# Performance work log

Measured on AMD Instinct MI355X. Metric: run time of the kernel, lower is better.

## Reference

```python
import jax, jax.numpy as jnp
import numpy as np
import math

B, T, C = 4, 2048, 1024
H = 16
D = C // H

def setup_inputs() -> dict:
    key = jax.random.key(0)
    k1, k2, k3 = jax.random.split(key, 3)
    x = jax.random.normal(k1, (B, T, C), dtype=jnp.float32)
    w_attn = jax.random.normal(k2, (3 * C, C), dtype=jnp.float32) * (1.0 / math.sqrt(C))
    b_attn = jnp.zeros((3 * C,), dtype=jnp.float32)
    w_proj = jax.random.normal(k3, (C, C), dtype=jnp.float32) * (1.0 / math.sqrt(C))
    b_proj = jnp.zeros((C,), dtype=jnp.float32)
    return {"x": x, "w_attn": w_attn, "b_attn": b_attn, "w_proj": w_proj, "b_proj": b_proj}

def reference(x, w_attn, b_attn, w_proj, b_proj):
    Bq, Tq, Cq = x.shape
    qkv = x @ w_attn.T + b_attn                      # [B,T,3C]
    q, k, v = jnp.split(qkv, 3, axis=-1)
    q = q.reshape(Bq, Tq, H, D).transpose(0, 2, 1, 3)  # [B,H,T,D]
    k = k.reshape(Bq, Tq, H, D).transpose(0, 2, 1, 3)
    v = v.reshape(Bq, Tq, H, D).transpose(0, 2, 1, 3)
    att = jnp.einsum('bhqd,bhkd->bhqk', q, k) * (1.0 / math.sqrt(D))
    causal = jnp.tril(jnp.ones((Tq, Tq), dtype=bool))
    att = jnp.where(causal[None, None], att, -jnp.inf)
    att = jax.nn.softmax(att, axis=-1)
    y = jnp.einsum('bhqk,bhkd->bhqd', att, v)          # [B,H,T,D]
    y = y.transpose(0, 2, 1, 3).reshape(Bq, Tq, Cq)
    return y @ w_proj.T + b_proj
```

## Files before the change

### kernel.cpp

```cpp
#include <hip/hip_runtime.h>
#include <hip/hip_bf16.h>


typedef __hip_bfloat16 bf16;
typedef __attribute__((ext_vector_type(8))) short bf16x8;
typedef __attribute__((ext_vector_type(4))) float f32x4;
typedef __attribute__((ext_vector_type(16))) float f32x16;

#define MFMA16(a, b, c) __builtin_amdgcn_mfma_f32_16x16x32_bf16(a, b, c, 0, 0, 0)
#define MFMA32(a, b, c) __builtin_amdgcn_mfma_f32_32x32x16_bf16(a, b, c, 0, 0, 0)
#define GLOAD_LDS(g, l) __builtin_amdgcn_global_load_lds( \
    (const __attribute__((address_space(1))) void*)(g),    \
    (__attribute__((address_space(3))) void*)(l), 16, 0, 0)

constexpr int Bn = 4, Tn = 2048, Cn = 1024, Hn = 16, Dn = 64;
constexpr size_t HT_ELEMS = (size_t)64 * Tn * Dn;
constexpr float QSCALE = 0.18033688011112042f;

__device__ __forceinline__ short f2bf(float f) {
    unsigned u = __float_as_uint(f);
    return (short)((u + 0x7FFF + ((u >> 16) & 1)) >> 16);
}
__device__ __forceinline__ bf16 bfbits(short s) { bf16 b; __builtin_memcpy(&b, &s, 2); return b; }

__device__ __forceinline__ unsigned cvtpk_bf16(float lo, float hi) {
    unsigned r;
    asm("v_cvt_pk_bf16_f32 %0, %1, %2" : "=v"(r) : "v"(lo), "v"(hi));
    return r;
}
__device__ __forceinline__ void permswap(unsigned& a, unsigned& b) {
#if __has_builtin(__builtin_amdgcn_permlane32_swap)
    auto r = __builtin_amdgcn_permlane32_swap(a, b, false, false);
    a = (unsigned)r[0]; b = (unsigned)r[1];
#else
    asm("v_permlane32_swap_b32 %0, %1" : "+v"(a), "+v"(b));
#endif
}
__device__ __forceinline__ bf16x8 pack4(unsigned w0, unsigned w1, unsigned w2, unsigned w3) {
    union { unsigned u[4]; bf16x8 v; } t;
    t.u[0] = w0; t.u[1] = w1; t.u[2] = w2; t.u[3] = w3;
    return t.v;
}

__global__ __launch_bounds__(256) void cast3_kernel(
    const float* __restrict__ x, const float* __restrict__ wa,
    const float* __restrict__ wp, bf16* __restrict__ out)
{
    size_t i = (size_t)blockIdx.x * 256 + threadIdx.x;
    const float* src; size_t off;
    if (i < 1048576)      { src = x;  off = i; }
    else if (i < 1441792) { src = wa; off = i - 1048576; }
    else                  { src = wp; off = i - 1441792; }
    const float4* p = (const float4*)(src + off * 8);
    float4 a = p[0], b = p[1];
    bf16x8 r;
    r[0] = f2bf(a.x); r[1] = f2bf(a.y); r[2] = f2bf(a.z); r[3] = f2bf(a.w);
    r[4] = f2bf(b.x); r[5] = f2bf(b.y); r[6] = f2bf(b.z); r[7] = f2bf(b.w);
    *(bf16x8*)(out + i * 8) = r;
}

__global__ __launch_bounds__(256) void qkv_gemm128(
    const bf16* __restrict__ Am, const bf16* __restrict__ Wm,
    const float* __restrict__ bias,
    bf16* __restrict__ qo, bf16* __restrict__ ko, bf16* __restrict__ vo)
{
    constexpr int K = 1024;
    __shared__ bf16 As[4096], Bs[4096];
    const int tid = threadIdx.x;
    const int lane = tid & 63, w = tid >> 6;
    const int row = lane & 15, quad = lane >> 4;
    const int tn = blockIdx.x % 24, tm = blockIdx.x / 24;
    const int m0 = tm * 128, n0 = tn * 128;

    const int srow = tid >> 2, skch = tid & 3;
    const bf16* ag0 = Am + (size_t)(m0 + srow) * K + skch * 8;
    const bf16* ag1 = ag0 + (size_t)64 * K;
    const bf16* wg0 = Wm + (size_t)(n0 + srow) * K + skch * 8;
    const bf16* wg1 = wg0 + (size_t)64 * K;
    bf16* asl0 = As + tid * 8;  bf16* asl1 = As + 2048 + tid * 8;
    bf16* bsl0 = Bs + tid * 8;  bf16* bsl1 = Bs + 2048 + tid * 8;

    f32x4 acc[4][4];
    #pragma unroll
    for (int i = 0; i < 4; i++)
        #pragma unroll
        for (int j = 0; j < 4; j++) acc[i][j] = {0, 0, 0, 0};

    const int r0 = (w >> 1) * 64, c0 = (w & 1) * 64;

    for (int k0 = 0; k0 < K; k0 += 32) {
        __syncthreads();
        GLOAD_LDS(ag0 + k0, asl0);
        GLOAD_LDS(ag1 + k0, asl1);
        GLOAD_LDS(wg0 + k0, bsl0);
        GLOAD_LDS(wg1 + k0, bsl1);
        __syncthreads();
        bf16x8 af[4], bfv[4];
        #pragma unroll
        for (int it = 0; it < 4; it++)
            af[it] = *(const bf16x8*)(As + (r0 + it * 16 + row) * 32 + quad * 8);
        #pragma unroll
        for (int jt = 0; jt < 4; jt++)
            bfv[jt] = *(const bf16x8*)(Bs + (c0 + jt * 16 + row) * 32 + quad * 8);
        #pragma unroll
        for (int it = 0; it < 4; it++)
            #pragma unroll
            for (int jt = 0; jt < 4; jt++)
                acc[it][jt] = MFMA16(af[it], bfv[jt], acc[it][jt]);
    }

    #pragma unroll
    for (int it = 0; it < 4; it++)
    #pragma unroll
    for (int jt = 0; jt < 4; jt++)
    #pragma unroll
    for (int r = 0; r < 4; r++) {
        int m = m0 + r0 + it * 16 + quad * 4 + r;
        int n = n0 + c0 + jt * 16 + row;
        float val = acc[it][jt][r] + bias[n];
        int which = n >> 10, cc = n & 1023;
        if (which == 0) val *= QSCALE;
        bf16 bv = bfbits(f2bf(val));
        int h = cc >> 6, d = cc & 63;
        int b = m >> 11, t = m & 2047;
        int bh = b * Hn + h;
        if (which == 0)      qo[((size_t)bh * Tn + t) * Dn + d] = bv;
        else if (which == 1) ko[((size_t)bh * Tn + t) * Dn + d] = bv;
        else                 vo[((size_t)bh * 64 + (t >> 5)) * 2048 + (size_t)d * 32 + (t & 31)] = bv;
    }
}

__global__ __launch_bounds__(256, 4) void attn_kernel(
    const bf16* __restrict__ qbp, const bf16* __restrict__ kbp,
    const bf16* __restrict__ vtb, bf16* __restrict__ ob,
    unsigned* __restrict__ counters)
{
    __shared__ __align__(128) bf16 SB[4][2048];
    __shared__ float lbufw[4][32];
    __shared__ unsigned item_s;
    const int tid  = threadIdx.x;
    const int lane = tid & 63;
    const int w    = tid >> 6;
    const int l31  = lane & 31, hl = lane >> 5;
    const int qid  = blockIdx.x & 7;
    unsigned* ctr  = counters + qid * 32;

    const int stage_off = w * 1024 + (lane >> 3) * 128
                        + (((lane & 7) ^ ((lane >> 3) & 7)) << 4);
    const int kxor = (l31 & 7) << 4;
    const int sxor = ((l31 >> 1) & 7) << 4;

    for (;;) {
        if (tid == 0) item_s = atomicAdd(ctr, 1u);
        __syncthreads();
        const unsigned item = item_s;
        if (item >= 128u) break;
        const int qb8  = 15 - (int)(item >> 3);
        const int bh   = qid * 8 + (int)(item & 7);
        const int jmax = qb8 * 4 + 3;
        const int qtw  = qb8 * 4 + w;
        const int q0w  = qtw * 32;

        const bf16* Q  = qbp + (size_t)bh * Tn * Dn;
        const char* Kh = (const char*)(kbp + (size_t)bh * Tn * Dn);
        const char* Vh = (const char*)vtb + (size_t)bh * 262144;

        bf16x8 bQ[4];
        {
            const bf16* qp = Q + (size_t)(q0w + l31) * Dn + hl * 8;
            #pragma unroll
            for (int kf = 0; kf < 4; kf++) bQ[kf] = *(const bf16x8*)(qp + kf * 16);
        }

        f32x16 o2[2];
        o2[0] = {0,0,0,0,0,0,0,0,0,0,0,0,0,0,0,0};
        o2[1] = {0,0,0,0,0,0,0,0,0,0,0,0,0,0,0,0};
        float lsum = 0.f;

        GLOAD_LDS(Kh + stage_off, (char*)SB[0] + w * 1024);
        GLOAD_LDS(Vh + stage_off, (char*)SB[2] + w * 1024);
        __syncthreads();

        for (int j = 0; j <= jmax; j++) {
            const int cur = j & 1;
            if (j < jmax) {
                const int nb = cur ^ 1;
                GLOAD_LDS(Kh + (size_t)(j + 1) * 4096 + stage_off, (char*)SB[nb] + w * 1024);
                GLOAD_LDS(Vh + (size_t)(j + 1) * 4096 + stage_off, (char*)SB[2 + nb] + w * 1024);
            }
            if (j <= qtw) {
                const char* KB = (const char*)SB[cur];
                const char* VB = (const char*)SB[2 + cur];
                bf16x8 aK[4];
                #pragma unroll
                for (int kf = 0; kf < 4; kf++)
                    aK[kf] = *(const bf16x8*)(KB + l31 * 128 + ((((kf * 2 + hl)) << 4) ^ kxor));

                f32x16 s = {0,0,0,0,0,0,0,0,0,0,0,0,0,0,0,0};
                __builtin_amdgcn_s_setprio(1);
                s = MFMA32(aK[0], bQ[0], s);
                s = MFMA32(aK[1], bQ[1], s);
                s = MFMA32(aK[2], bQ[2], s);
                s = MFMA32(aK[3], bQ[3], s);
                __builtin_amdgcn_s_setprio(0);

                bf16x8 vf[4];
                #pragma unroll
                for (int i2 = 0; i2 < 4; i2++) {
                    const int vh = i2 >> 1, kc = i2 & 1;
                    const int stripe = vh * 16 + (l31 >> 1);
                    vf[i2] = *(const bf16x8*)(VB + stripe * 128
                              + ((((l31 & 1) * 4 + kc * 2 + hl) << 4) ^ sxor));
                }

                float p[16];
                if (j == qtw) {
                    #pragma unroll
                    for (int r = 0; r < 16; r++) {
                        const int krow = (r & 3) + 8 * (r >> 2) + 4 * hl;
                        float e = exp2f(s[r]);
                        p[r] = (krow > l31) ? 0.f : e;
                    }
                } else {
                    #pragma unroll
                    for (int r = 0; r < 16; r++) p[r] = exp2f(s[r]);
                }
                lsum += (((p[0]+p[1]) + (p[2]+p[3])) + ((p[4]+p[5]) + (p[6]+p[7])))
                      + (((p[8]+p[9]) + (p[10]+p[11])) + ((p[12]+p[13]) + (p[14]+p[15])));

                unsigned a0 = cvtpk_bf16(p[0],  p[1]),  b0 = cvtpk_bf16(p[4],  p[5]);
                unsigned a1 = cvtpk_bf16(p[2],  p[3]),  b1 = cvtpk_bf16(p[6],  p[7]);
                unsigned a2 = cvtpk_bf16(p[8],  p[9]),  b2 = cvtpk_bf16(p[12], p[13]);
                unsigned a3 = cvtpk_bf16(p[10], p[11]), b3 = cvtpk_bf16(p[14], p[15]);
                permswap(a0, b0);
                permswap(a1, b1);
                permswap(a2, b2);
                permswap(a3, b3);
                const bf16x8 P0 = pack4(a0, a1, b0, b1);
                const bf16x8 P1 = pack4(a2, a3, b2, b3);

                __builtin_amdgcn_s_setprio(1);
                o2[0] = MFMA32(P0, vf[0], o2[0]);
                o2[0] = MFMA32(P1, vf[1], o2[0]);
                o2[1] = MFMA32(P0, vf[2], o2[1]);
                o2[1] = MFMA32(P1, vf[3], o2[1]);
                __builtin_amdgcn_s_setprio(0);
            }
            __syncthreads();
        }

        unsigned lsu = __float_as_uint(lsum), lsv = lsu;
        permswap(lsu, lsv);
        const float ltot = __uint_as_float(lsu) + __uint_as_float(lsv);
        if (hl == 0) lbufw[w][l31] = 1.0f / ltot;
        asm volatile("s_waitcnt lgkmcnt(0)" ::: "memory");

        char* obl = (char*)SB[w];
        #pragma unroll
        for (int r = 0; r < 16; r++) {
            const int q  = (r & 3) + 8 * (r >> 2) + 4 * hl;
            const float rl = lbufw[w][q];
            const int qx = (q & 7) << 4;
            *(short*)(obl + q * 128 + ((2 * l31) ^ qx))      = f2bf(o2[0][r] * rl);
            *(short*)(obl + q * 128 + ((64 + 2 * l31) ^ qx)) = f2bf(o2[1][r] * rl);
        }
        asm volatile("s_waitcnt lgkmcnt(0)" ::: "memory");

        {
            const int q = lane >> 1, half = lane & 1;
            const int qx = (q & 7) << 4;
            const int b = bh >> 4, h = bh & 15;
            bf16* gdst = ob + ((size_t)(b * Tn + (q0w + q))) * Cn + h * Dn + half * 32;
            #pragma unroll
            for (int c = 0; c < 4; c++) {
                bf16x8 rv = *(const bf16x8*)(obl + q * 128 + (((half * 64) + c * 16) ^ qx));
                *(bf16x8*)(gdst + c * 8) = rv;
            }
        }
        __syncthreads();
    }
}

__global__ __launch_bounds__(256) void proj_gemm128(
    const bf16* __restrict__ Am, const bf16* __restrict__ Wm,
    const float* __restrict__ bias, float* __restrict__ out)
{
    constexpr int K = 1024;
    __shared__ bf16 As[4096], Bs[4096];
    const int tid = threadIdx.x;
    const int lane = tid & 63, w = tid >> 6;
    const int row = lane & 15, quad = lane >> 4;
    const int tn = blockIdx.x % 8, tm = blockIdx.x / 8;
    const int m0 = tm * 128, n0 = tn * 128;

    const int srow = tid >> 2, skch = tid & 3;
    const bf16* ag0 = Am + (size_t)(m0 + srow) * K + skch * 8;
    const bf16* ag1 = ag0 + (size_t)64 * K;
    const bf16* wg0 = Wm + (size_t)(n0 + srow) * K + skch * 8;
    const bf16* wg1 = wg0 + (size_t)64 * K;
    bf16* asl0 = As + tid * 8;  bf16* asl1 = As + 2048 + tid * 8;
    bf16* bsl0 = Bs + tid * 8;  bf16* bsl1 = Bs + 2048 + tid * 8;

    f32x4 acc[4][4];
    #pragma unroll
    for (int i = 0; i < 4; i++)
        #pragma unroll
        for (int j = 0; j < 4; j++) acc[i][j] = {0, 0, 0, 0};

    const int r0 = (w >> 1) * 64, c0 = (w & 1) * 64;

    for (int k0 = 0; k0 < K; k0 += 32) {
        __syncthreads();
        GLOAD_LDS(ag0 + k0, asl0);
        GLOAD_LDS(ag1 + k0, asl1);
        GLOAD_LDS(wg0 + k0, bsl0);
        GLOAD_LDS(wg1 + k0, bsl1);
        __syncthreads();
        bf16x8 af[4], bfv[4];
        #pragma unroll
        for (int it = 0; it < 4; it++)
            af[it] = *(const bf16x8*)(As + (r0 + it * 16 + row) * 32 + quad * 8);
        #pragma unroll
        for (int jt = 0; jt < 4; jt++)
            bfv[jt] = *(const bf16x8*)(Bs + (c0 + jt * 16 + row) * 32 + quad * 8);
        #pragma unroll
        for (int it = 0; it < 4; it++)
            #pragma unroll
            for (int jt = 0; jt < 4; jt++)
                acc[it][jt] = MFMA16(af[it], bfv[jt], acc[it][jt]);
    }

    #pragma unroll
    for (int it = 0; it < 4; it++)
    #pragma unroll
    for (int jt = 0; jt < 4; jt++)
    #pragma unroll
    for (int r = 0; r < 4; r++) {
        int m = m0 + r0 + it * 16 + quad * 4 + r;
        int n = n0 + c0 + jt * 16 + row;
        out[(size_t)m * 1024 + n] = acc[it][jt][r] + bias[n];
    }
}

extern "C" void kernel_launch(void* const* d_in, const int* in_sizes, int n_in,
                              void* d_out, int out_size, void* d_ws, size_t ws_size,
                              hipStream_t stream) {
    const float* x      = (const float*)d_in[0];
    const float* w_attn = (const float*)d_in[1];
    const float* b_attn = (const float*)d_in[2];
    const float* w_proj = (const float*)d_in[3];
    const float* b_proj = (const float*)d_in[4];
    float* out = (float*)d_out;

    unsigned* counters = (unsigned*)d_ws;
    bf16* ws  = (bf16*)((char*)d_ws + 1024);
    bf16* xb  = ws;
    bf16* wab = xb  + (size_t)8192 * 1024;
    bf16* wpb = wab + (size_t)3072 * 1024;
    bf16* q   = wpb + (size_t)1024 * 1024;
    bf16* k   = q  + HT_ELEMS;
    bf16* vt  = k  + HT_ELEMS;
    bf16* o   = vt + HT_ELEMS;

    hipMemsetAsync(counters, 0, 1024, stream);

    cast3_kernel<<<6144, 256, 0, stream>>>(x, w_attn, w_proj, xb);

    qkv_gemm128 <<<64 * 24, 256, 0, stream>>>(xb, wab, b_attn, q, k, vt);
    attn_kernel <<<1024, 256, 0, stream>>>(q, k, vt, o, counters);
    proj_gemm128<<<64 * 8, 256, 0, stream>>>(o, wpb, b_proj, out);
}
```

Before: 304.7 us.

## Double-buffer LDS tiles and swizzle block order in QKV and projection GEMMs

Both GEMM kernels now keep two LDS buffers, prefetching the next K-slice with global_load_lds while MFMAs consume the current one. This cuts the k-loop from two barriers to one and is meant to overlap memory latency with compute. Block indices are also remapped with an XCD-style swizzle (bid&7 groups) to improve L2 locality across the MI355X chiplets. LDS use doubles, which may lower occupancy, and the async-load completion ordering relies on the single barrier at the end of each iteration.

```diff
diff --git a/kernel.cpp b/kernel.cpp
--- a/kernel.cpp
+++ b/kernel.cpp
@@ -65,11 +65,13 @@
     bf16* __restrict__ qo, bf16* __restrict__ ko, bf16* __restrict__ vo)
 {
     constexpr int K = 1024;
-    __shared__ bf16 As[4096], Bs[4096];
+    __shared__ bf16 As[2][4096], Bs[2][4096];
     const int tid = threadIdx.x;
     const int lane = tid & 63, w = tid >> 6;
     const int row = lane & 15, quad = lane >> 4;
-    const int tn = blockIdx.x % 24, tm = blockIdx.x / 24;
+    const unsigned bid = blockIdx.x;
+    const unsigned swz = (bid & 7) * 192 + (bid >> 3);
+    const int tn = swz % 24, tm = swz / 24;
     const int m0 = tm * 128, n0 = tn * 128;
 
     const int srow = tid >> 2, skch = tid & 3;
@@ -77,8 +79,6 @@
     const bf16* ag1 = ag0 + (size_t)64 * K;
     const bf16* wg0 = Wm + (size_t)(n0 + srow) * K + skch * 8;
     const bf16* wg1 = wg0 + (size_t)64 * K;
-    bf16* asl0 = As + tid * 8;  bf16* asl1 = As + 2048 + tid * 8;
-    bf16* bsl0 = Bs + tid * 8;  bf16* bsl1 = Bs + 2048 + tid * 8;
 
     f32x4 acc[4][4];
     #pragma unroll
@@ -88,25 +88,37 @@
 
     const int r0 = (w >> 1) * 64, c0 = (w & 1) * 64;
 
+    GLOAD_LDS(ag0, As[0] + tid * 8);
+    GLOAD_LDS(ag1, As[0] + 2048 + tid * 8);
+    GLOAD_LDS(wg0, Bs[0] + tid * 8);
+    GLOAD_LDS(wg1, Bs[0] + 2048 + tid * 8);
+    __syncthreads();
+
+    int cur = 0;
     for (int k0 = 0; k0 < K; k0 += 32) {
-        __syncthreads();
-        GLOAD_LDS(ag0 + k0, asl0);
-        GLOAD_LDS(ag1 + k0, asl1);
-        GLOAD_LDS(wg0 + k0, bsl0);
-        GLOAD_LDS(wg1 + k0, bsl1);
-        __syncthreads();
+        const int nb = cur ^ 1;
+        if (k0 + 32 < K) {
+            GLOAD_LDS(ag0 + k0 + 32, As[nb] + tid * 8);
+            GLOAD_LDS(ag1 + k0 + 32, As[nb] + 2048 + tid * 8);
+            GLOAD_LDS(wg0 + k0 + 32, Bs[nb] + tid * 8);
+            GLOAD_LDS(wg1 + k0 + 32, Bs[nb] + 2048 + tid * 8);
+        }
+        const bf16* Ac = As[cur];
+        const bf16* Bc = Bs[cur];
         bf16x8 af[4], bfv[4];
         #pragma unroll
         for (int it = 0; it < 4; it++)
-            af[it] = *(const bf16x8*)(As + (r0 + it * 16 + row) * 32 + quad * 8);
+            af[it] = *(const bf16x8*)(Ac + (r0 + it * 16 + row) * 32 + quad * 8);
         #pragma unroll
         for (int jt = 0; jt < 4; jt++)
-            bfv[jt] = *(const bf16x8*)(Bs + (c0 + jt * 16 + row) * 32 + quad * 8);
+            bfv[jt] = *(const bf16x8*)(Bc + (c0 + jt * 16 + row) * 32 + quad * 8);
         #pragma unroll
         for (int it = 0; it < 4; it++)
             #pragma unroll
             for (int jt = 0; jt < 4; jt++)
                 acc[it][jt] = MFMA16(af[it], bfv[jt], acc[it][jt]);
+        __syncthreads();
+        cur = nb;
     }
 
     #pragma unroll
@@ -286,11 +298,13 @@
     const float* __restrict__ bias, float* __restrict__ out)
 {
     constexpr int K = 1024;
-    __shared__ bf16 As[4096], Bs[4096];
+    __shared__ bf16 As[2][4096], Bs[2][4096];
     const int tid = threadIdx.x;
     const int lane = tid & 63, w = tid >> 6;
     const int row = lane & 15, quad = lane >> 4;
-    const int tn = blockIdx.x % 8, tm = blockIdx.x / 8;
+    const unsigned bid = blockIdx.x;
+    const unsigned swz = (bid & 7) * 64 + (bid >> 3);
+    const int tn = swz % 8, tm = swz / 8;
     const int m0 = tm * 128, n0 = tn * 128;
 
     const int srow = tid >> 2, skch = tid & 3;
@@ -298,8 +312,6 @@
     const bf16* ag1 = ag0 + (size_t)64 * K;
     const bf16* wg0 = Wm + (size_t)(n0 + srow) * K + skch * 8;
     const bf16* wg1 = wg0 + (size_t)64 * K;
-    bf16* asl0 = As + tid * 8;  bf16* asl1 = As + 2048 + tid * 8;
-    bf16* bsl0 = Bs + tid * 8;  bf16* bsl1 = Bs + 2048 + tid * 8;
 
     f32x4 acc[4][4];
     #pragma unroll
@@ -309,25 +321,37 @@
 
     const int r0 = (w >> 1) * 64, c0 = (w & 1) * 64;
 
+    GLOAD_LDS(ag0, As[0] + tid * 8);
+    GLOAD_LDS(ag1, As[0] + 2048 + tid * 8);
+    GLOAD_LDS(wg0, Bs[0] + tid * 8);
+    GLOAD_LDS(wg1, Bs[0] + 2048 + tid * 8);
+    __syncthreads();
+
+    int cur = 0;
     for (int k0 = 0; k0 < K; k0 += 32) {
-        __syncthreads();
-        GLOAD_LDS(ag0 + k0, asl0);
-        GLOAD_LDS(ag1 + k0, asl1);
-        GLOAD_LDS(wg0 + k0, bsl0);
-        GLOAD_LDS(wg1 + k0, bsl1);
-        __syncthreads();
+        const int nb = cur ^ 1;
+        if (k0 + 32 < K) {
+            GLOAD_LDS(ag0 + k0 + 32, As[nb] + tid * 8);
+            GLOAD_LDS(ag1 + k0 + 32, As[nb] + 2048 + tid * 8);
+            GLOAD_LDS(wg0 + k0 + 32, Bs[nb] + tid * 8);
+            GLOAD_LDS(wg1 + k0 + 32, Bs[nb] + 2048 + tid * 8);
+        }
+        const bf16* Ac = As[cur];
+        const bf16* Bc = Bs[cur];
         bf16x8 af[4], bfv[4];
         #pragma unroll
         for (int it = 0; it < 4; it++)
-            af[it] = *(const bf16x8*)(As + (r0 + it * 16 + row) * 32 + quad * 8);
+            af[it] = *(const bf16x8*)(Ac + (r0 + it * 16 + row) * 32 + quad * 8);
         #pragma unroll
         for (int jt = 0; jt < 4; jt++)
-            bfv[jt] = *(const bf16x8*)(Bs + (c0 + jt * 16 + row) * 32 + quad * 8);
+            bfv[jt] = *(const bf16x8*)(Bc + (c0 + jt * 16 + row) * 32 + quad * 8);
         #pragma unroll
         for (int it = 0; it < 4; it++)
             #pragma unroll
             for (int jt = 0; jt < 4; jt++)
                 acc[it][jt] = MFMA16(af[it], bfv[jt], acc[it][jt]);
+        __syncthreads();
+        cur = nb;
     }
 
     #pragma unroll
```

After: 287.2 us. 5.7% less time.

## Replace atomic work queue with static paired causal tiles and XCD-aware block remap

Applied to the files above, without the earlier changes.

The attention kernel no longer takes work items from atomic counters. Each of 512 blocks now handles a fixed pair of query tiles (pair and 15-pair) for one head, which balances the causal workload statically and removes both the memset and the per-item atomics and syncs. Both GEMMs remap block indices so that blocks sharing the low 3 bits (likely the same XCD under round-robin dispatch) work on contiguous tiles, aiming for better L2 reuse. The static schedule gives up the dynamic load balancing the queue provided, and the new attention grid of 512 blocks may leave compute units underused if occupancy is limited.

```diff
diff --git a/kernel.cpp b/kernel.cpp
--- a/kernel.cpp
+++ b/kernel.cpp
@@ -69,7 +69,10 @@
     const int tid = threadIdx.x;
     const int lane = tid & 63, w = tid >> 6;
     const int row = lane & 15, quad = lane >> 4;
-    const int tn = blockIdx.x % 24, tm = blockIdx.x / 24;
+    const unsigned bid = blockIdx.x;
+    const int x8 = bid & 7, l = bid >> 3;
+    const int tm = (x8 >> 1) * 16 + l / 12;
+    const int tn = (x8 & 1) * 12 + l % 12;
     const int m0 = tm * 128, n0 = tn * 128;
 
     const int srow = tid >> 2, skch = tid & 3;
@@ -132,38 +135,35 @@
 
 __global__ __launch_bounds__(256, 4) void attn_kernel(
     const bf16* __restrict__ qbp, const bf16* __restrict__ kbp,
-    const bf16* __restrict__ vtb, bf16* __restrict__ ob,
-    unsigned* __restrict__ counters)
+    const bf16* __restrict__ vtb, bf16* __restrict__ ob)
 {
     __shared__ __align__(128) bf16 SB[4][2048];
     __shared__ float lbufw[4][32];
-    __shared__ unsigned item_s;
     const int tid  = threadIdx.x;
     const int lane = tid & 63;
     const int w    = tid >> 6;
     const int l31  = lane & 31, hl = lane >> 5;
-    const int qid  = blockIdx.x & 7;
-    unsigned* ctr  = counters + qid * 32;
+    const int bid  = blockIdx.x;
+    const int qid  = bid & 7;
+    const int idx  = bid >> 3;
+    const int bh   = qid * 8 + (idx & 7);
+    const int pair = idx >> 3;
 
     const int stage_off = w * 1024 + (lane >> 3) * 128
                         + (((lane & 7) ^ ((lane >> 3) & 7)) << 4);
     const int kxor = (l31 & 7) << 4;
     const int sxor = ((l31 >> 1) & 7) << 4;
 
-    for (;;) {
-        if (tid == 0) item_s = atomicAdd(ctr, 1u);
-        __syncthreads();
-        const unsigned item = item_s;
-        if (item >= 128u) break;
-        const int qb8  = 15 - (int)(item >> 3);
-        const int bh   = qid * 8 + (int)(item & 7);
+    const bf16* Q  = qbp + (size_t)bh * Tn * Dn;
+    const char* Kh = (const char*)(kbp + (size_t)bh * Tn * Dn);
+    const char* Vh = (const char*)vtb + (size_t)bh * 262144;
+
+    #pragma unroll 1
+    for (int sub = 0; sub < 2; sub++) {
+        const int qb8  = sub ? (15 - pair) : pair;
         const int jmax = qb8 * 4 + 3;
         const int qtw  = qb8 * 4 + w;
         const int q0w  = qtw * 32;
-
-        const bf16* Q  = qbp + (size_t)bh * Tn * Dn;
-        const char* Kh = (const char*)(kbp + (size_t)bh * Tn * Dn);
-        const char* Vh = (const char*)vtb + (size_t)bh * 262144;
 
         bf16x8 bQ[4];
         {
@@ -290,7 +290,10 @@
     const int tid = threadIdx.x;
     const int lane = tid & 63, w = tid >> 6;
     const int row = lane & 15, quad = lane >> 4;
-    const int tn = blockIdx.x % 8, tm = blockIdx.x / 8;
+    const unsigned bid = blockIdx.x;
+    const int x8 = bid & 7, l = bid >> 3;
+    const int tm = x8 * 8 + l / 8;
+    const int tn = l % 8;
     const int m0 = tm * 128, n0 = tn * 128;
 
     const int srow = tid >> 2, skch = tid & 3;
@@ -352,7 +355,6 @@
     const float* b_proj = (const float*)d_in[4];
     float* out = (float*)d_out;
 
-    unsigned* counters = (unsigned*)d_ws;
     bf16* ws  = (bf16*)((char*)d_ws + 1024);
     bf16* xb  = ws;
     bf16* wab = xb  + (size_t)8192 * 1024;
@@ -362,11 +364,9 @@
     bf16* vt  = k  + HT_ELEMS;
     bf16* o   = vt + HT_ELEMS;
 
-    hipMemsetAsync(counters, 0, 1024, stream);
-
     cast3_kernel<<<6144, 256, 0, stream>>>(x, w_attn, w_proj, xb);
 
     qkv_gemm128 <<<64 * 24, 256, 0, stream>>>(xb, wab, b_attn, q, k, vt);
-    attn_kernel <<<1024, 256, 0, stream>>>(q, k, vt, o, counters);
+    attn_kernel <<<512, 256, 0, stream>>>(q, k, vt, o);
     proj_gemm128<<<64 * 8, 256, 0, stream>>>(o, wpb, b_proj, out);
 }
```

After: 296.7 us. 2.6% less time.
